# Kernel optimization log

Hardware: AMD Instinct MI355X
Metric: run time of the kernel (lower is better)

The kernel has to match this reference:

```python
import jax, jax.numpy as jnp
import numpy as np

B, L, D, H = 4, 1024, 768, 6
DH = D // H
EPS = 1e-5


def setup_inputs() -> dict:
    key = jax.random.key(0)
    kq, kk, kv, kl, kw = jax.random.split(key, 5)
    Q = jax.random.normal(kq, (B, L, D), jnp.float32)
    K = jax.random.normal(kk, (B, L, D), jnp.float32)
    V = jax.random.normal(kv, (B, L, D), jnp.float32)
    # realistic padding: each batch element has a valid length in [L//2, L]
    lengths = jax.random.randint(kl, (B,), L // 2, L + 1)
    valid = jnp.arange(L)[None, :] < lengths[:, None]          # (B, L)
    pad_mask = valid[:, :, None] & valid[:, None, :]           # (B, L, L), True = keep
    bx_packed = ~valid                                         # (B, L), True = padded
    # BatchNorm affine params (per-head channels)
    g1 = jnp.ones((H,), jnp.float32)
    b1 = jnp.zeros((H,), jnp.float32)
    g2 = jnp.ones((H,), jnp.float32)
    b2 = jnp.zeros((H,), jnp.float32)
    # posterior gate: Linear(H, 2)
    Wp = jax.random.normal(kw, (2, H), jnp.float32) * (1.0 / np.sqrt(H))
    bp = jnp.zeros((2,), jnp.float32)
    return {"Q": Q, "K": K, "V": V, "pad_mask": pad_mask, "bx_packed": bx_packed,
            "g1": g1, "b1": b1, "g2": g2, "b2": b2, "Wp": Wp, "bp": bp}


def _split_heads(x):
    b, l, _ = x.shape
    return x.reshape(b, l, H, DH).transpose(0, 2, 1, 3)  # (B, H, L, DH)


def _batchnorm(x, g, b):
    # x: (B, H, N); training-mode BatchNorm1d over channels H (stats over B and N)
    m = x.mean(axis=(0, 2), keepdims=True)
    v = x.var(axis=(0, 2), keepdims=True)  # biased, as torch uses for normalization
    return (x - m) * jax.lax.rsqrt(v + EPS) * g[None, :, None] + b[None, :, None]


def _remove_nan(x):
    return jnp.where(jnp.isnan(x), jnp.zeros_like(x), x)


def reference(Q, K, V, pad_mask, bx_packed, g1, b1, g2, b2, Wp, bp):
    Qh, Kh, Vh = _split_heads(Q), _split_heads(K), _split_heads(V)
    b, h, l, _ = Qh.shape
    # DistMatrix: negative squared Euclidean distance between query/key vectors
    # scores[b,h,i,j] = -||Q_i - K_j||^2, via the GEMM-friendly expansion
    q2 = jnp.sum(Qh * Qh, axis=-1)                     # (B, H, L)
    k2 = jnp.sum(Kh * Kh, axis=-1)                     # (B, H, L)
    qk = jnp.einsum("bhid,bhjd->bhij", Qh, Kh)         # (B, H, L, L)
    co = -(q2[..., :, None] + k2[..., None, :] - 2.0 * qk)
    # norm1 over flattened L*L
    co = _batchnorm(co.reshape(b, h, l * l), g1, b1).reshape(b, h, l, l)
    # zero out positions where pad_mask is False (in-place masked fill in torch)
    co = jnp.where(pad_mask[:, None, :, :], co, 0.0)
    co = jax.nn.softmax(co, axis=-1)
    co = _remove_nan(co)
    # column-sum attention mass per key position
    w = co.sum(axis=-2)                                # (B, H, L)
    w = _batchnorm(w, g2, b2).transpose(0, 2, 1)       # (B, L, H)
    # posterior gate: Linear(H,2) + softmax, take class-0 probability
    w = jax.nn.softmax(w @ Wp.T + bp, axis=-1)[..., 0]  # (B, L)
    w = _remove_nan(w)
    w = jnp.where(bx_packed, -jnp.inf, w)
    w = jax.nn.softmax(w, axis=-1)
    w = _remove_nan(w)[..., None]                      # (B, L, 1)
    return co, w, Vh
```

## Files before the change

### kernel.cpp

```cpp
#include <hip/hip_runtime.h>
#include <stdint.h>
#include <stddef.h>

#define BB 4
#define LL 1024
#define DD 768
#define HH 6
#define DHH 128
#define EPS 1e-5f

#define CO_ELEMS 25165824
#define W_ELEMS  4096

#define OFF_Q2  0
#define OFF_K2  24576
#define OFF_WC  49152
#define OFF_SP  73728
#define OFF_AC  79872
#define OFF_SS  79888
#define OFF_WP  81920
#define OFF_GP  1654784
#define OFF_MS1 5193728
#define OFF_MS2 5242880

typedef __attribute__((ext_vector_type(8))) short short8;
typedef __attribute__((ext_vector_type(4))) float f32x4;

__device__ __forceinline__ short8 ld_bf8(const float* __restrict__ p) {
    const float4 a = *(const float4*)(p);
    const float4 b = *(const float4*)(p + 4);
    short8 r;
    r[0] = (short)(__float_as_uint(a.x) >> 16);
    r[1] = (short)(__float_as_uint(a.y) >> 16);
    r[2] = (short)(__float_as_uint(a.z) >> 16);
    r[3] = (short)(__float_as_uint(a.w) >> 16);
    r[4] = (short)(__float_as_uint(b.x) >> 16);
    r[5] = (short)(__float_as_uint(b.y) >> 16);
    r[6] = (short)(__float_as_uint(b.z) >> 16);
    r[7] = (short)(__float_as_uint(b.w) >> 16);
    return r;
}

__global__ void k_vh(const float* __restrict__ V, float* __restrict__ out) {
    int cid = blockIdx.x * 256 + threadIdx.x;
    if (cid >= 786432) return;
    int d4 = cid & 31;
    int rest = cid >> 5;
    int l = rest & 1023;
    int bh = rest >> 10;
    int b = bh / HH, h = bh - b * HH;
    f32x4 v = *(const f32x4*)(V + (size_t)(b * LL + l) * DD + h * DHH + d4 * 4);
    __builtin_nontemporal_store(v, (f32x4*)(out + (size_t)cid * 4));
}

__global__ __launch_bounds__(256) void k_gram(
        const float* __restrict__ Q, const float* __restrict__ K,
        float* __restrict__ ws, float* __restrict__ gramP,
        float* __restrict__ ms1, float* __restrict__ ms2) {
    const int ic = blockIdx.x;
    const int bh = blockIdx.y;
    const int which = blockIdx.z;
    const int b = bh / HH, h = bh - b * HH;
    const float* src = (which ? K : Q) + (size_t)b * LL * DD + h * DHH;
    float* sqout = ws + (which ? OFF_K2 : OFF_Q2) + bh * 1024 + ic * 128;

    const int t = threadIdx.x, lane = t & 63, wv = t >> 6;
    const int lm = lane & 15, quad = lane >> 4;

    __shared__ float tileT[128][129];
    __shared__ float q2loc[128];

    const int ig = t >> 5;
    const int d0 = (t & 31) * 4;
#pragma unroll 4
    for (int p = 0; p < 16; p++) {
        const int i_loc = p * 8 + ig;
        float4 v = *(const float4*)(src + (size_t)(ic * 128 + i_loc) * DD + d0);
        tileT[d0 + 0][i_loc] = __uint_as_float(__float_as_uint(v.x) & 0xffff0000u);
        tileT[d0 + 1][i_loc] = __uint_as_float(__float_as_uint(v.y) & 0xffff0000u);
        tileT[d0 + 2][i_loc] = __uint_as_float(__float_as_uint(v.z) & 0xffff0000u);
        tileT[d0 + 3][i_loc] = __uint_as_float(__float_as_uint(v.w) & 0xffff0000u);
        float s = v.x * v.x + v.y * v.y + v.z * v.z + v.w * v.w;
#pragma unroll
        for (int off = 1; off < 32; off <<= 1) s += __shfl_xor(s, off);
        if ((t & 31) == 0) { q2loc[i_loc] = s; sqout[i_loc] = s; }
    }
    __syncthreads();

    if (t < 128) {
        float s1 = 0.f, s2 = 0.f;
#pragma unroll 8
        for (int i = 0; i < 128; i++) {
            float v = tileT[t][i];
            s1 += v;
            s2 += v * q2loc[i];
        }
        const size_t mo = ((size_t)(which * 24 + bh) * 8 + ic) * 128 + t;
        ms1[mo] = s1;
        ms2[mo] = s2;
    }

    const size_t gbase = ((size_t)(which * 24 + bh) * 8 + ic) * 9216;
    int pi = 0;
    for (int dt = 0; dt < 8; dt++) {
        for (int et = dt; et < 8; et++, pi++) {
            if ((pi & 3) != wv) continue;
            f32x4 acc = (f32x4)(0.0f);
#pragma unroll
            for (int kk = 0; kk < 4; kk++) {
                const int i0 = kk * 32 + quad * 8;
                const float* pa = &tileT[dt * 16 + lm][i0];
                const float* pb = &tileT[et * 16 + lm][i0];
                short8 af, bf;
#pragma unroll
                for (int e = 0; e < 8; e++) {
                    af[e] = (short)(__float_as_uint(pa[e]) >> 16);
                    bf[e] = (short)(__float_as_uint(pb[e]) >> 16);
                }
                acc = __builtin_amdgcn_mfma_f32_16x16x32_bf16(af, bf, acc, 0, 0, 0);
            }
            if (dt != et && which == 0) {
                acc[0] *= 2.f; acc[1] *= 2.f; acc[2] *= 2.f; acc[3] *= 2.f;
            }
            *(f32x4*)&gramP[gbase + (size_t)pi * 256 + lane * 4] = acc;
        }
    }
}

__global__ __launch_bounds__(256) void k_stats3(
        const float* __restrict__ ms1, const float* __restrict__ ms2,
        const float* __restrict__ gramP,
        const float* __restrict__ q2, const float* __restrict__ k2,
        float* __restrict__ statsP) {
    const int bh = blockIdx.x;
    const int t = threadIdx.x, lane = t & 63, w = t >> 6;
    __shared__ float sQ[128], sK[128], sQq2[128], sKk2[128];
    __shared__ float sred[4][4];
    __shared__ float gred[4];

    {
        const int d = t & 127, which = t >> 7;
        const float* p1 = ms1 + (size_t)(which * 24 + bh) * 1024 + d;
        const float* p2 = ms2 + (size_t)(which * 24 + bh) * 1024 + d;
        float s1 = 0.f, s2 = 0.f;
#pragma unroll
        for (int ic = 0; ic < 8; ic++) { s1 += p1[ic * 128]; s2 += p2[ic * 128]; }
        if (which) { sK[d] = s1; sKk2[d] = s2; }
        else       { sQ[d] = s1; sQq2[d] = s2; }
    }
    {
        f32x4 qv = *(const f32x4*)(q2 + bh * 1024 + t * 4);
        f32x4 kv = *(const f32x4*)(k2 + bh * 1024 + t * 4);
        float p0 = qv[0] + qv[1] + qv[2] + qv[3];
        float p1 = qv[0]*qv[0] + qv[1]*qv[1] + qv[2]*qv[2] + qv[3]*qv[3];
        float p2 = kv[0] + kv[1] + kv[2] + kv[3];
        float p3 = kv[0]*kv[0] + kv[1]*kv[1] + kv[2]*kv[2] + kv[3]*kv[3];
#pragma unroll
        for (int off = 1; off < 64; off <<= 1) {
            p0 += __shfl_xor(p0, off); p1 += __shfl_xor(p1, off);
            p2 += __shfl_xor(p2, off); p3 += __shfl_xor(p3, off);
        }
        if (lane == 0) { sred[w][0] = p0; sred[w][1] = p1; sred[w][2] = p2; sred[w][3] = p3; }
    }
    {
        const float* gq = gramP + (size_t)(0 * 24 + bh) * 8 * 9216;
        const float* gk = gramP + (size_t)(1 * 24 + bh) * 8 * 9216;
        float gg = 0.f;
        for (int pi = 0; pi < 36; pi++) {
            const size_t o = (size_t)pi * 256 + t;
            float a = 0.f, c = 0.f;
#pragma unroll
            for (int icc = 0; icc < 8; icc++) {
                a += gq[(size_t)icc * 9216 + o];
                c += gk[(size_t)icc * 9216 + o];
            }
            gg += a * c;
        }
#pragma unroll
        for (int off = 1; off < 64; off <<= 1) gg += __shfl_xor(gg, off);
        if (lane == 0) gred[w] = gg;
    }
    __syncthreads();
    if (t < 64) {
        float dA  = sQ[t] * sK[t] + sQ[t + 64] * sK[t + 64];
        float dBq = sQq2[t] * sK[t] + sQq2[t + 64] * sK[t + 64];
        float dBk = sQ[t] * sKk2[t] + sQ[t + 64] * sKk2[t + 64];
#pragma unroll
        for (int off = 1; off < 64; off <<= 1) {
            dA += __shfl_xor(dA, off); dBq += __shfl_xor(dBq, off); dBk += __shfl_xor(dBk, off);
        }
        if (t == 0) {
            float SQ2   = sred[0][0] + sred[1][0] + sred[2][0] + sred[3][0];
            float SQ2SQ = sred[0][1] + sred[1][1] + sred[2][1] + sred[3][1];
            float SK2   = sred[0][2] + sred[1][2] + sred[2][2] + sred[3][2];
            float SK2SQ = sred[0][3] + sred[1][3] + sred[2][3] + sred[3][3];
            float GG = gred[0] + gred[1] + gred[2] + gred[3];
            float sumS  = 2.f * dA - 1024.f * (SQ2 + SK2);
            float sumS2 = 4.f * GG + 1024.f * (SQ2SQ + SK2SQ) + 2.f * SQ2 * SK2 - 4.f * (dBq + dBk);
            statsP[bh * 2]     = sumS;
            statsP[bh * 2 + 1] = sumS2;
        }
    }
}

__global__ void k_stats2(const float* __restrict__ statsP,
                         const float* __restrict__ g1, const float* __restrict__ b1,
                         float* __restrict__ ac) {
    const int t = threadIdx.x;
    if (t < HH) {
        float T1 = 0.f, T2 = 0.f;
#pragma unroll
        for (int b = 0; b < 4; b++) {
            T1 += statsP[(b * HH + t) * 2];
            T2 += statsP[(b * HH + t) * 2 + 1];
        }
        const float N = 4194304.f;
        float m_ = T1 / N;
        float var = fmaxf(T2 / N - m_ * m_, 0.0f);
        float r = rsqrtf(var + EPS);
        float a = r * g1[t];
        ac[t] = a;
        ac[8 + t] = b1[t] - m_ * a;
    }
}

__global__ __launch_bounds__(512, 1) void k_fused(
        const float* __restrict__ Q, const float* __restrict__ Km,
        const float* __restrict__ q2, const float* __restrict__ k2,
        const float* __restrict__ ac, const unsigned char* __restrict__ bx,
        float* __restrict__ co, float* __restrict__ wcolP) {
    const int bh = blockIdx.x;
    const int strip = blockIdx.y;
    const int b = bh / HH, h = bh - b * HH;
    const int t = threadIdx.x, lane = t & 63, w = t >> 6;
    const int lm = lane & 15, quad = lane >> 4;
    const int i0 = strip * 32;
    const int jw = w * 128;

    __shared__ float e_lds[32][1028];
    __shared__ float rowsum[32];
    if (t < 32) rowsum[t] = 0.f;
    __syncthreads();

    const float* Qb = Q + (size_t)b * LL * DD + h * DHH;
    const float* Kb = Km + (size_t)b * LL * DD + h * DHH;
    const float a1 = ac[h], c1 = ac[8 + h];
    const unsigned char* bxb = bx + b * LL;

    short8 qf[2][4];
#pragma unroll
    for (int s = 0; s < 2; s++)
#pragma unroll
        for (int kk = 0; kk < 4; kk++)
            qf[s][kk] = ld_bf8(Qb + (size_t)(i0 + s * 16 + lm) * DD + kk * 32 + quad * 8);

    bool vi[2];
    float q2v[2];
#pragma unroll
    for (int s = 0; s < 2; s++) {
        vi[s] = (bxb[i0 + s * 16 + lm] == 0);
        q2v[s] = q2[bh * 1024 + i0 + s * 16 + lm];
    }

    float rsum0 = 0.f, rsum1 = 0.f;
#pragma unroll
    for (int jt = 0; jt < 8; jt++) {
        const int jb = jw + jt * 16;
        short8 kf[4];
#pragma unroll
        for (int kk = 0; kk < 4; kk++)
            kf[kk] = ld_bf8(Kb + (size_t)(jb + lm) * DD + kk * 32 + quad * 8);
        f32x4 acc0 = (f32x4)(0.0f), acc1 = (f32x4)(0.0f);
#pragma unroll
        for (int kk = 0; kk < 4; kk++) {
            acc0 = __builtin_amdgcn_mfma_f32_16x16x32_bf16(kf[kk], qf[0][kk], acc0, 0, 0, 0);
            acc1 = __builtin_amdgcn_mfma_f32_16x16x32_bf16(kf[kk], qf[1][kk], acc1, 0, 0, 0);
        }
        const f32x4 k2v = *(const f32x4*)(k2 + bh * 1024 + jb + quad * 4);
        const uchar4 m4 = *(const uchar4*)(bxb + jb + quad * 4);
        const bool vj0 = (m4.x == 0), vj1 = (m4.y == 0), vj2 = (m4.z == 0), vj3 = (m4.w == 0);
        {
            f32x4 ev;
            ev[0] = (vi[0] && vj0) ? __expf(fminf(a1 * (2.0f * acc0[0] - q2v[0] - k2v[0]) + c1, 60.0f)) : 1.0f;
            ev[1] = (vi[0] && vj1) ? __expf(fminf(a1 * (2.0f * acc0[1] - q2v[0] - k2v[1]) + c1, 60.0f)) : 1.0f;
            ev[2] = (vi[0] && vj2) ? __expf(fminf(a1 * (2.0f * acc0[2] - q2v[0] - k2v[2]) + c1, 60.0f)) : 1.0f;
            ev[3] = (vi[0] && vj3) ? __expf(fminf(a1 * (2.0f * acc0[3] - q2v[0] - k2v[3]) + c1, 60.0f)) : 1.0f;
            *(f32x4*)&e_lds[lm][jb + quad * 4] = ev;
            rsum0 += (ev[0] + ev[1]) + (ev[2] + ev[3]);
        }
        {
            f32x4 ev;
            ev[0] = (vi[1] && vj0) ? __expf(fminf(a1 * (2.0f * acc1[0] - q2v[1] - k2v[0]) + c1, 60.0f)) : 1.0f;
            ev[1] = (vi[1] && vj1) ? __expf(fminf(a1 * (2.0f * acc1[1] - q2v[1] - k2v[1]) + c1, 60.0f)) : 1.0f;
            ev[2] = (vi[1] && vj2) ? __expf(fminf(a1 * (2.0f * acc1[2] - q2v[1] - k2v[2]) + c1, 60.0f)) : 1.0f;
            ev[3] = (vi[1] && vj3) ? __expf(fminf(a1 * (2.0f * acc1[3] - q2v[1] - k2v[3]) + c1, 60.0f)) : 1.0f;
            *(f32x4*)&e_lds[16 + lm][jb + quad * 4] = ev;
            rsum1 += (ev[0] + ev[1]) + (ev[2] + ev[3]);
        }
    }
    rsum0 += __shfl_xor(rsum0, 16);
    rsum0 += __shfl_xor(rsum0, 32);
    rsum1 += __shfl_xor(rsum1, 16);
    rsum1 += __shfl_xor(rsum1, 32);
    if (lane < 16) {
        atomicAdd(&rowsum[lm], rsum0);
        atomicAdd(&rowsum[16 + lm], rsum1);
    }
    __syncthreads();

    const int cg = t & 255, rh = t >> 8;
    float* cob = co + ((size_t)bh << 20) + (size_t)(i0 + rh * 16) * 1024 + cg * 4;
    float* wp = wcolP + ((size_t)((strip * 2 + rh) * 24 + bh)) * 1024 + cg * 4;
    float cs0 = 0.f, cs1 = 0.f, cs2 = 0.f, cs3 = 0.f;
#pragma unroll
    for (int rr = 0; rr < 16; rr++) {
        const int r = rh * 16 + rr;
        const float inv = 1.0f / rowsum[r];
        f32x4 v = *(const f32x4*)&e_lds[r][cg * 4];
        v[0] *= inv; v[1] *= inv; v[2] *= inv; v[3] *= inv;
        __builtin_nontemporal_store(v, (f32x4*)(cob + (size_t)rr * 1024));
        cs0 += v[0]; cs1 += v[1]; cs2 += v[2]; cs3 += v[3];
    }
    f32x4 wv; wv[0] = cs0; wv[1] = cs1; wv[2] = cs2; wv[3] = cs3;
    *(f32x4*)wp = wv;
}

__global__ void k_wcol_reduce(const float* __restrict__ wcolP,
                              float* __restrict__ wcol, float* __restrict__ ws2) {
    const int t = threadIdx.x;
    int g = blockIdx.x * 256 + t;
    float s = 0.f;
#pragma unroll 8
    for (int strip = 0; strip < 64; strip++)
        s += wcolP[(size_t)strip * 24576 + g];
    wcol[g] = s;
    float a = s, b = s * s;
#pragma unroll
    for (int off = 1; off < 64; off <<= 1) { a += __shfl_xor(a, off); b += __shfl_xor(b, off); }
    __shared__ float sc[4][2];
    if ((t & 63) == 0) { sc[t >> 6][0] = a; sc[t >> 6][1] = b; }
    __syncthreads();
    if (t == 0) {
        ws2[blockIdx.x * 2]     = sc[0][0] + sc[1][0] + sc[2][0] + sc[3][0];
        ws2[blockIdx.x * 2 + 1] = sc[0][1] + sc[1][1] + sc[2][1] + sc[3][1];
    }
}

__global__ __launch_bounds__(1024) void k_tail(
        const float* __restrict__ wcol, const float* __restrict__ ws2,
        const unsigned char* __restrict__ bx,
        const float* __restrict__ g2, const float* __restrict__ b2,
        const float* __restrict__ Wp, const float* __restrict__ bp,
        float* __restrict__ wout) {
    const int t = threadIdx.x, lane = t & 63, wv = t >> 6;
    __shared__ float abuf[12];
    __shared__ float xb[4096];
    __shared__ float wred[16][2];

    if (t < HH) {
        float s = 0.f, s2 = 0.f;
        for (int b = 0; b < 4; b++) {
            int bh = b * HH + t;
#pragma unroll
            for (int sub = 0; sub < 4; sub++) {
                int blk = bh * 4 + sub;
                s += ws2[blk * 2];
                s2 += ws2[blk * 2 + 1];
            }
        }
        float m = s / 4096.f;
        float var = fmaxf(s2 / 4096.f - m * m, 0.0f);
        float r = rsqrtf(var + EPS);
        float a = r * g2[t];
        abuf[t] = a;
        abuf[6 + t] = b2[t] - m * a;
    }
    __syncthreads();

    const float bp0 = bp[0], bp1 = bp[1];
#pragma unroll
    for (int p = 0; p < 4; p++) {
        int idx = t + p * 1024;
        int b = idx >> 10, l = idx & 1023;
        float z0 = bp0, z1 = bp1;
#pragma unroll
        for (int h = 0; h < HH; h++) {
            float wn = abuf[h] * wcol[(size_t)(b * HH + h) * 1024 + l] + abuf[6 + h];
            z0 += wn * Wp[h];
            z1 += wn * Wp[HH + h];
        }
        float pc = 1.0f / (1.0f + __expf(z1 - z0));
        xb[idx] = bx[b * LL + l] ? -INFINITY : pc;
    }
    __syncthreads();

    const int bb = t >> 8, tb = t & 255;
    float4 xv = *(const float4*)&xb[bb * 1024 + tb * 4];
    float mx = fmaxf(fmaxf(xv.x, xv.y), fmaxf(xv.z, xv.w));
#pragma unroll
    for (int off = 1; off < 64; off <<= 1) mx = fmaxf(mx, __shfl_xor(mx, off));
    if (lane == 0) wred[wv][0] = mx;
    __syncthreads();
    mx = fmaxf(fmaxf(wred[bb * 4][0], wred[bb * 4 + 1][0]),
               fmaxf(wred[bb * 4 + 2][0], wred[bb * 4 + 3][0]));
    float e0 = __expf(xv.x - mx), e1 = __expf(xv.y - mx);
    float e2 = __expf(xv.z - mx), e3 = __expf(xv.w - mx);
    float ss = e0 + e1 + e2 + e3;
#pragma unroll
    for (int off = 1; off < 64; off <<= 1) ss += __shfl_xor(ss, off);
    if (lane == 0) wred[wv][1] = ss;
    __syncthreads();
    float sum = wred[bb * 4][1] + wred[bb * 4 + 1][1] + wred[bb * 4 + 2][1] + wred[bb * 4 + 3][1];
    float4 o;
    o.x = e0 / sum; o.y = e1 / sum; o.z = e2 / sum; o.w = e3 / sum;
    *(float4*)&wout[bb * 1024 + tb * 4] = o;
}

extern "C" void kernel_launch(void* const* d_in, const int* in_sizes, int n_in,
                              void* d_out, int out_size, void* d_ws, size_t ws_size,
                              hipStream_t stream) {
    const float* Q  = (const float*)d_in[0];
    const float* K  = (const float*)d_in[1];
    const float* V  = (const float*)d_in[2];
    const unsigned char* bx = (const unsigned char*)d_in[4];
    const float* g1 = (const float*)d_in[5];
    const float* b1 = (const float*)d_in[6];
    const float* g2 = (const float*)d_in[7];
    const float* b2 = (const float*)d_in[8];
    const float* Wp = (const float*)d_in[9];
    const float* bp = (const float*)d_in[10];

    float* out  = (float*)d_out;
    float* co   = out;
    float* wout = out + CO_ELEMS;
    float* vh   = out + CO_ELEMS + W_ELEMS;

    float* ws = (float*)d_ws;
    float* q2     = ws + OFF_Q2;
    float* k2     = ws + OFF_K2;
    float* wcol   = ws + OFF_WC;
    float* statsP = ws + OFF_SP;
    float* ac     = ws + OFF_AC;
    float* ws2    = ws + OFF_SS;
    float* wcolP  = ws + OFF_WP;
    float* gramP  = ws + OFF_GP;
    float* ms1    = ws + OFF_MS1;
    float* ms2    = ws + OFF_MS2;

    k_gram<<<dim3(8, 24, 2), 256, 0, stream>>>(Q, K, ws, gramP, ms1, ms2);
    k_vh<<<3072, 256, 0, stream>>>(V, vh);
    k_stats3<<<24, 256, 0, stream>>>(ms1, ms2, gramP, q2, k2, statsP);
    k_stats2<<<1, 64, 0, stream>>>(statsP, g1, b1, ac);
    k_fused<<<dim3(24, 32), 512, 0, stream>>>(Q, K, q2, k2, ac, bx, co, wcolP);
    k_wcol_reduce<<<96, 256, 0, stream>>>(wcolP, wcol, ws2);
    k_tail<<<1, 1024, 0, stream>>>(wcol, ws2, bx, g2, b2, Wp, bp, wout);
}
```

Before: 269.9 us.

## Fold V head split into gram kernel, widen stats, persist fused kernel with K prefetch

The separate V head-split kernel is merged into k_gram as a third z-slice, which removes one launch. k_stats3 moves to 1024 threads so the gram-product reduction is spread across more waves. k_fused becomes a 256-block grid in which each block handles three (bh, strip) tiles in turn, fitting all 768 tiles into a single wave of blocks. Inside, it double-buffers the K fragment loads in registers and switches to exp2 with precomputed log2e-scaled constants and FMA. The risks are the extra per-block serialisation and the higher register pressure from the prefetch buffers.

```diff
diff --git a/kernel.cpp b/kernel.cpp
--- a/kernel.cpp
+++ b/kernel.cpp
@@ -8,6 +8,7 @@
 #define HH 6
 #define DHH 128
 #define EPS 1e-5f
+#define LOG2E 1.44269504088896f
 
 #define CO_ELEMS 25165824
 #define W_ELEMS  4096
@@ -41,30 +42,48 @@
     return r;
 }
 
-__global__ void k_vh(const float* __restrict__ V, float* __restrict__ out) {
-    int cid = blockIdx.x * 256 + threadIdx.x;
-    if (cid >= 786432) return;
-    int d4 = cid & 31;
-    int rest = cid >> 5;
-    int l = rest & 1023;
-    int bh = rest >> 10;
-    int b = bh / HH, h = bh - b * HH;
-    f32x4 v = *(const f32x4*)(V + (size_t)(b * LL + l) * DD + h * DHH + d4 * 4);
-    __builtin_nontemporal_store(v, (f32x4*)(out + (size_t)cid * 4));
+__device__ __forceinline__ short8 pack_bf8(float4 a, float4 b) {
+    short8 r;
+    r[0] = (short)(__float_as_uint(a.x) >> 16);
+    r[1] = (short)(__float_as_uint(a.y) >> 16);
+    r[2] = (short)(__float_as_uint(a.z) >> 16);
+    r[3] = (short)(__float_as_uint(a.w) >> 16);
+    r[4] = (short)(__float_as_uint(b.x) >> 16);
+    r[5] = (short)(__float_as_uint(b.y) >> 16);
+    r[6] = (short)(__float_as_uint(b.z) >> 16);
+    r[7] = (short)(__float_as_uint(b.w) >> 16);
+    return r;
 }
 
 __global__ __launch_bounds__(256) void k_gram(
         const float* __restrict__ Q, const float* __restrict__ K,
+        const float* __restrict__ V,
         float* __restrict__ ws, float* __restrict__ gramP,
-        float* __restrict__ ms1, float* __restrict__ ms2) {
+        float* __restrict__ ms1, float* __restrict__ ms2,
+        float* __restrict__ vh) {
     const int ic = blockIdx.x;
     const int bh = blockIdx.y;
     const int which = blockIdx.z;
     const int b = bh / HH, h = bh - b * HH;
+    const int t = threadIdx.x;
+
+    if (which == 2) {
+        const float* srcv = V + (size_t)b * LL * DD + h * DHH;
+        float* dstv = vh + ((size_t)bh * LL + (size_t)ic * 128) * DHH;
+#pragma unroll
+        for (int p = 0; p < 16; p++) {
+            const int idx = p * 256 + t;
+            const int row = idx >> 5, d4 = idx & 31;
+            f32x4 v = *(const f32x4*)(srcv + (size_t)(ic * 128 + row) * DD + d4 * 4);
+            __builtin_nontemporal_store(v, (f32x4*)(dstv + (size_t)row * DHH + d4 * 4));
+        }
+        return;
+    }
+
     const float* src = (which ? K : Q) + (size_t)b * LL * DD + h * DHH;
     float* sqout = ws + (which ? OFF_K2 : OFF_Q2) + bh * 1024 + ic * 128;
 
-    const int t = threadIdx.x, lane = t & 63, wv = t >> 6;
+    const int lane = t & 63, wv = t >> 6;
     const int lm = lane & 15, quad = lane >> 4;
 
     __shared__ float tileT[128][129];
@@ -127,7 +146,7 @@
     }
 }
 
-__global__ __launch_bounds__(256) void k_stats3(
+__global__ __launch_bounds__(1024) void k_stats3(
         const float* __restrict__ ms1, const float* __restrict__ ms2,
         const float* __restrict__ gramP,
         const float* __restrict__ q2, const float* __restrict__ k2,
@@ -135,10 +154,10 @@
     const int bh = blockIdx.x;
     const int t = threadIdx.x, lane = t & 63, w = t >> 6;
     __shared__ float sQ[128], sK[128], sQq2[128], sKk2[128];
-    __shared__ float sred[4][4];
-    __shared__ float gred[4];
-
-    {
+    __shared__ float sred[16][4];
+    __shared__ float gred[16];
+
+    if (t < 256) {
         const int d = t & 127, which = t >> 7;
         const float* p1 = ms1 + (size_t)(which * 24 + bh) * 1024 + d;
         const float* p2 = ms2 + (size_t)(which * 24 + bh) * 1024 + d;
@@ -148,9 +167,10 @@
         if (which) { sK[d] = s1; sKk2[d] = s2; }
         else       { sQ[d] = s1; sQq2[d] = s2; }
     }
-    {
-        f32x4 qv = *(const f32x4*)(q2 + bh * 1024 + t * 4);
-        f32x4 kv = *(const f32x4*)(k2 + bh * 1024 + t * 4);
+    if (t >= 512 && t < 768) {
+        const int tt = t - 512;
+        f32x4 qv = *(const f32x4*)(q2 + bh * 1024 + tt * 4);
+        f32x4 kv = *(const f32x4*)(k2 + bh * 1024 + tt * 4);
         float p0 = qv[0] + qv[1] + qv[2] + qv[3];
         float p1 = qv[0]*qv[0] + qv[1]*qv[1] + qv[2]*qv[2] + qv[3]*qv[3];
         float p2 = kv[0] + kv[1] + kv[2] + kv[3];
@@ -166,13 +186,14 @@
         const float* gq = gramP + (size_t)(0 * 24 + bh) * 8 * 9216;
         const float* gk = gramP + (size_t)(1 * 24 + bh) * 8 * 9216;
         float gg = 0.f;
-        for (int pi = 0; pi < 36; pi++) {
-            const size_t o = (size_t)pi * 256 + t;
+#pragma unroll
+        for (int it = 0; it < 9; it++) {
+            const int f = it * 1024 + t;
             float a = 0.f, c = 0.f;
 #pragma unroll
             for (int icc = 0; icc < 8; icc++) {
-                a += gq[(size_t)icc * 9216 + o];
-                c += gk[(size_t)icc * 9216 + o];
+                a += gq[(size_t)icc * 9216 + f];
+                c += gk[(size_t)icc * 9216 + f];
             }
             gg += a * c;
         }
@@ -190,11 +211,13 @@
             dA += __shfl_xor(dA, off); dBq += __shfl_xor(dBq, off); dBk += __shfl_xor(dBk, off);
         }
         if (t == 0) {
-            float SQ2   = sred[0][0] + sred[1][0] + sred[2][0] + sred[3][0];
-            float SQ2SQ = sred[0][1] + sred[1][1] + sred[2][1] + sred[3][1];
-            float SK2   = sred[0][2] + sred[1][2] + sred[2][2] + sred[3][2];
-            float SK2SQ = sred[0][3] + sred[1][3] + sred[2][3] + sred[3][3];
-            float GG = gred[0] + gred[1] + gred[2] + gred[3];
+            float SQ2   = sred[8][0] + sred[9][0] + sred[10][0] + sred[11][0];
+            float SQ2SQ = sred[8][1] + sred[9][1] + sred[10][1] + sred[11][1];
+            float SK2   = sred[8][2] + sred[9][2] + sred[10][2] + sred[11][2];
+            float SK2SQ = sred[8][3] + sred[9][3] + sred[10][3] + sred[11][3];
+            float GG = 0.f;
+#pragma unroll
+            for (int i = 0; i < 16; i++) GG += gred[i];
             float sumS  = 2.f * dA - 1024.f * (SQ2 + SK2);
             float sumS2 = 4.f * GG + 1024.f * (SQ2SQ + SK2SQ) + 2.f * SQ2 * SK2 - 4.f * (dBq + dBk);
             statsP[bh * 2]     = sumS;
@@ -229,100 +252,130 @@
         const float* __restrict__ q2, const float* __restrict__ k2,
         const float* __restrict__ ac, const unsigned char* __restrict__ bx,
         float* __restrict__ co, float* __restrict__ wcolP) {
-    const int bh = blockIdx.x;
-    const int strip = blockIdx.y;
-    const int b = bh / HH, h = bh - b * HH;
+    const int g = blockIdx.x;
     const int t = threadIdx.x, lane = t & 63, w = t >> 6;
     const int lm = lane & 15, quad = lane >> 4;
-    const int i0 = strip * 32;
     const int jw = w * 128;
 
     __shared__ float e_lds[32][1028];
-    __shared__ float rowsum[32];
-    if (t < 32) rowsum[t] = 0.f;
-    __syncthreads();
-
-    const float* Qb = Q + (size_t)b * LL * DD + h * DHH;
-    const float* Kb = Km + (size_t)b * LL * DD + h * DHH;
-    const float a1 = ac[h], c1 = ac[8 + h];
-    const unsigned char* bxb = bx + b * LL;
-
-    short8 qf[2][4];
-#pragma unroll
-    for (int s = 0; s < 2; s++)
-#pragma unroll
-        for (int kk = 0; kk < 4; kk++)
-            qf[s][kk] = ld_bf8(Qb + (size_t)(i0 + s * 16 + lm) * DD + kk * 32 + quad * 8);
-
-    bool vi[2];
-    float q2v[2];
-#pragma unroll
-    for (int s = 0; s < 2; s++) {
-        vi[s] = (bxb[i0 + s * 16 + lm] == 0);
-        q2v[s] = q2[bh * 1024 + i0 + s * 16 + lm];
-    }
-
-    float rsum0 = 0.f, rsum1 = 0.f;
-#pragma unroll
-    for (int jt = 0; jt < 8; jt++) {
-        const int jb = jw + jt * 16;
-        short8 kf[4];
-#pragma unroll
-        for (int kk = 0; kk < 4; kk++)
-            kf[kk] = ld_bf8(Kb + (size_t)(jb + lm) * DD + kk * 32 + quad * 8);
-        f32x4 acc0 = (f32x4)(0.0f), acc1 = (f32x4)(0.0f);
+    __shared__ float rowsum[3][32];
+    if (t < 96) ((float*)rowsum)[t] = 0.f;
+    __syncthreads();
+
+#pragma unroll 1
+    for (int rep = 0; rep < 3; rep++) {
+        const int f = g * 3 + rep;
+        const int bh = f >> 5, strip = f & 31;
+        const int b = bh / HH, h = bh - b * HH;
+        const int i0 = strip * 32;
+        const float* Qb = Q + (size_t)b * LL * DD + h * DHH;
+        const float* Kb = Km + (size_t)b * LL * DD + h * DHH;
+        const float a1 = ac[h], c1 = ac[8 + h];
+        const unsigned char* bxb = bx + b * LL;
+        const float a1l = a1 * LOG2E;
+        const float a2l = 2.0f * a1l;
+        const float c1l = c1 * LOG2E;
+
+        short8 qf[2][4];
+#pragma unroll
+        for (int s = 0; s < 2; s++)
+#pragma unroll
+            for (int kk = 0; kk < 4; kk++)
+                qf[s][kk] = ld_bf8(Qb + (size_t)(i0 + s * 16 + lm) * DD + kk * 32 + quad * 8);
+
+        bool vi0, vi1;
+        float cr0, cr1;
+        {
+            vi0 = (bxb[i0 + lm] == 0);
+            vi1 = (bxb[i0 + 16 + lm] == 0);
+            cr0 = c1l - a1l * q2[bh * 1024 + i0 + lm];
+            cr1 = c1l - a1l * q2[bh * 1024 + i0 + 16 + lm];
+        }
+
+        float4 raw[2][8];
 #pragma unroll
         for (int kk = 0; kk < 4; kk++) {
-            acc0 = __builtin_amdgcn_mfma_f32_16x16x32_bf16(kf[kk], qf[0][kk], acc0, 0, 0, 0);
-            acc1 = __builtin_amdgcn_mfma_f32_16x16x32_bf16(kf[kk], qf[1][kk], acc1, 0, 0, 0);
-        }
-        const f32x4 k2v = *(const f32x4*)(k2 + bh * 1024 + jb + quad * 4);
-        const uchar4 m4 = *(const uchar4*)(bxb + jb + quad * 4);
-        const bool vj0 = (m4.x == 0), vj1 = (m4.y == 0), vj2 = (m4.z == 0), vj3 = (m4.w == 0);
-        {
-            f32x4 ev;
-            ev[0] = (vi[0] && vj0) ? __expf(fminf(a1 * (2.0f * acc0[0] - q2v[0] - k2v[0]) + c1, 60.0f)) : 1.0f;
-            ev[1] = (vi[0] && vj1) ? __expf(fminf(a1 * (2.0f * acc0[1] - q2v[0] - k2v[1]) + c1, 60.0f)) : 1.0f;
-            ev[2] = (vi[0] && vj2) ? __expf(fminf(a1 * (2.0f * acc0[2] - q2v[0] - k2v[2]) + c1, 60.0f)) : 1.0f;
-            ev[3] = (vi[0] && vj3) ? __expf(fminf(a1 * (2.0f * acc0[3] - q2v[0] - k2v[3]) + c1, 60.0f)) : 1.0f;
-            *(f32x4*)&e_lds[lm][jb + quad * 4] = ev;
-            rsum0 += (ev[0] + ev[1]) + (ev[2] + ev[3]);
-        }
-        {
-            f32x4 ev;
-            ev[0] = (vi[1] && vj0) ? __expf(fminf(a1 * (2.0f * acc1[0] - q2v[1] - k2v[0]) + c1, 60.0f)) : 1.0f;
-            ev[1] = (vi[1] && vj1) ? __expf(fminf(a1 * (2.0f * acc1[1] - q2v[1] - k2v[1]) + c1, 60.0f)) : 1.0f;
-            ev[2] = (vi[1] && vj2) ? __expf(fminf(a1 * (2.0f * acc1[2] - q2v[1] - k2v[2]) + c1, 60.0f)) : 1.0f;
-            ev[3] = (vi[1] && vj3) ? __expf(fminf(a1 * (2.0f * acc1[3] - q2v[1] - k2v[3]) + c1, 60.0f)) : 1.0f;
-            *(f32x4*)&e_lds[16 + lm][jb + quad * 4] = ev;
-            rsum1 += (ev[0] + ev[1]) + (ev[2] + ev[3]);
-        }
-    }
-    rsum0 += __shfl_xor(rsum0, 16);
-    rsum0 += __shfl_xor(rsum0, 32);
-    rsum1 += __shfl_xor(rsum1, 16);
-    rsum1 += __shfl_xor(rsum1, 32);
-    if (lane < 16) {
-        atomicAdd(&rowsum[lm], rsum0);
-        atomicAdd(&rowsum[16 + lm], rsum1);
-    }
-    __syncthreads();
-
-    const int cg = t & 255, rh = t >> 8;
-    float* cob = co + ((size_t)bh << 20) + (size_t)(i0 + rh * 16) * 1024 + cg * 4;
-    float* wp = wcolP + ((size_t)((strip * 2 + rh) * 24 + bh)) * 1024 + cg * 4;
-    float cs0 = 0.f, cs1 = 0.f, cs2 = 0.f, cs3 = 0.f;
-#pragma unroll
-    for (int rr = 0; rr < 16; rr++) {
-        const int r = rh * 16 + rr;
-        const float inv = 1.0f / rowsum[r];
-        f32x4 v = *(const f32x4*)&e_lds[r][cg * 4];
-        v[0] *= inv; v[1] *= inv; v[2] *= inv; v[3] *= inv;
-        __builtin_nontemporal_store(v, (f32x4*)(cob + (size_t)rr * 1024));
-        cs0 += v[0]; cs1 += v[1]; cs2 += v[2]; cs3 += v[3];
-    }
-    f32x4 wv; wv[0] = cs0; wv[1] = cs1; wv[2] = cs2; wv[3] = cs3;
-    *(f32x4*)wp = wv;
+            const float* p = Kb + (size_t)(jw + lm) * DD + kk * 32 + quad * 8;
+            raw[0][2 * kk]     = *(const float4*)(p);
+            raw[0][2 * kk + 1] = *(const float4*)(p + 4);
+        }
+
+        float rsum0 = 0.f, rsum1 = 0.f;
+#pragma unroll
+        for (int jt = 0; jt < 8; jt++) {
+            const int cur = jt & 1;
+            if (jt < 7) {
+                const int jb2 = jw + (jt + 1) * 16;
+#pragma unroll
+                for (int kk = 0; kk < 4; kk++) {
+                    const float* p = Kb + (size_t)(jb2 + lm) * DD + kk * 32 + quad * 8;
+                    raw[cur ^ 1][2 * kk]     = *(const float4*)(p);
+                    raw[cur ^ 1][2 * kk + 1] = *(const float4*)(p + 4);
+                }
+            }
+            short8 kf[4];
+#pragma unroll
+            for (int kk = 0; kk < 4; kk++)
+                kf[kk] = pack_bf8(raw[cur][2 * kk], raw[cur][2 * kk + 1]);
+            f32x4 acc0 = (f32x4)(0.0f), acc1 = (f32x4)(0.0f);
+#pragma unroll
+            for (int kk = 0; kk < 4; kk++) {
+                acc0 = __builtin_amdgcn_mfma_f32_16x16x32_bf16(kf[kk], qf[0][kk], acc0, 0, 0, 0);
+                acc1 = __builtin_amdgcn_mfma_f32_16x16x32_bf16(kf[kk], qf[1][kk], acc1, 0, 0, 0);
+            }
+            const int jb = jw + jt * 16;
+            const f32x4 k2v = *(const f32x4*)(k2 + bh * 1024 + jb + quad * 4);
+            const uchar4 m4 = *(const uchar4*)(bxb + jb + quad * 4);
+            const bool vj0 = (m4.x == 0), vj1 = (m4.y == 0), vj2 = (m4.z == 0), vj3 = (m4.w == 0);
+            f32x4 kc;
+            kc[0] = a1l * k2v[0]; kc[1] = a1l * k2v[1];
+            kc[2] = a1l * k2v[2]; kc[3] = a1l * k2v[3];
+            {
+                f32x4 ev;
+                ev[0] = (vi0 && vj0) ? exp2f(fminf(fmaf(a2l, acc0[0], cr0 - kc[0]), 86.56f)) : 1.0f;
+                ev[1] = (vi0 && vj1) ? exp2f(fminf(fmaf(a2l, acc0[1], cr0 - kc[1]), 86.56f)) : 1.0f;
+                ev[2] = (vi0 && vj2) ? exp2f(fminf(fmaf(a2l, acc0[2], cr0 - kc[2]), 86.56f)) : 1.0f;
+                ev[3] = (vi0 && vj3) ? exp2f(fminf(fmaf(a2l, acc0[3], cr0 - kc[3]), 86.56f)) : 1.0f;
+                *(f32x4*)&e_lds[lm][jb + quad * 4] = ev;
+                rsum0 += (ev[0] + ev[1]) + (ev[2] + ev[3]);
+            }
+            {
+                f32x4 ev;
+                ev[0] = (vi1 && vj0) ? exp2f(fminf(fmaf(a2l, acc1[0], cr1 - kc[0]), 86.56f)) : 1.0f;
+                ev[1] = (vi1 && vj1) ? exp2f(fminf(fmaf(a2l, acc1[1], cr1 - kc[1]), 86.56f)) : 1.0f;
+                ev[2] = (vi1 && vj2) ? exp2f(fminf(fmaf(a2l, acc1[2], cr1 - kc[2]), 86.56f)) : 1.0f;
+                ev[3] = (vi1 && vj3) ? exp2f(fminf(fmaf(a2l, acc1[3], cr1 - kc[3]), 86.56f)) : 1.0f;
+                *(f32x4*)&e_lds[16 + lm][jb + quad * 4] = ev;
+                rsum1 += (ev[0] + ev[1]) + (ev[2] + ev[3]);
+            }
+        }
+        rsum0 += __shfl_xor(rsum0, 16);
+        rsum0 += __shfl_xor(rsum0, 32);
+        rsum1 += __shfl_xor(rsum1, 16);
+        rsum1 += __shfl_xor(rsum1, 32);
+        if (lane < 16) {
+            atomicAdd(&rowsum[rep][lm], rsum0);
+            atomicAdd(&rowsum[rep][16 + lm], rsum1);
+        }
+        __syncthreads();
+
+        const int cg = t & 255, rh = t >> 8;
+        float* cob = co + ((size_t)bh << 20) + (size_t)(i0 + rh * 16) * 1024 + cg * 4;
+        float* wp = wcolP + ((size_t)((strip * 2 + rh) * 24 + bh)) * 1024 + cg * 4;
+        float cs0 = 0.f, cs1 = 0.f, cs2 = 0.f, cs3 = 0.f;
+#pragma unroll
+        for (int rr = 0; rr < 16; rr++) {
+            const int r = rh * 16 + rr;
+            const float inv = 1.0f / rowsum[rep][r];
+            f32x4 v = *(const f32x4*)&e_lds[r][cg * 4];
+            v[0] *= inv; v[1] *= inv; v[2] *= inv; v[3] *= inv;
+            __builtin_nontemporal_store(v, (f32x4*)(cob + (size_t)rr * 1024));
+            cs0 += v[0]; cs1 += v[1]; cs2 += v[2]; cs3 += v[3];
+        }
+        f32x4 wv; wv[0] = cs0; wv[1] = cs1; wv[2] = cs2; wv[3] = cs3;
+        *(f32x4*)wp = wv;
+        __syncthreads();
+    }
 }
 
 __global__ void k_wcol_reduce(const float* __restrict__ wcolP,
@@ -447,11 +500,10 @@
     float* ms1    = ws + OFF_MS1;
     float* ms2    = ws + OFF_MS2;
 
-    k_gram<<<dim3(8, 24, 2), 256, 0, stream>>>(Q, K, ws, gramP, ms1, ms2);
-    k_vh<<<3072, 256, 0, stream>>>(V, vh);
-    k_stats3<<<24, 256, 0, stream>>>(ms1, ms2, gramP, q2, k2, statsP);
+    k_gram<<<dim3(8, 24, 3), 256, 0, stream>>>(Q, K, V, ws, gramP, ms1, ms2, vh);
+    k_stats3<<<24, 1024, 0, stream>>>(ms1, ms2, gramP, q2, k2, statsP);
     k_stats2<<<1, 64, 0, stream>>>(statsP, g1, b1, ac);
-    k_fused<<<dim3(24, 32), 512, 0, stream>>>(Q, K, q2, k2, ac, bx, co, wcolP);
+    k_fused<<<256, 512, 0, stream>>>(Q, K, q2, k2, ac, bx, co, wcolP);
     k_wcol_reduce<<<96, 256, 0, stream>>>(wcolP, wcol, ws2);
     k_tail<<<1, 1024, 0, stream>>>(wcol, ws2, bx, g2, b2, Wp, bp, wout);
 }
```

Result: faster. 259.4 us (-3.9%).
